# Performance work log

Hardware: AMD Instinct MI355X
Metric: run time of the kernel (lower is better)

## Reference

```python
import jax, jax.numpy as jnp
import numpy as np

# --- config mirroring Prediction(__init__) ---
NUM_CLS = 3        # heatmap channels; total C = NUM_CLS + 2 (offset) + 2 (wh)
TOPK = 100         # peaks kept per stack output
SCALE = 4.0        # scale_factor: feature-map stride
CONF_TH = 0.1      # conf_th (also soft-NMS keep thresh, as in forward())
SIGMA = 0.5        # soft-NMS gaussian sigma (default in soft_nms_pytorch)


def setup_inputs() -> dict:
    key = jax.random.key(0)
    # network is identity => x is the raw head output (B, S, C, H, W)
    x = jax.random.normal(key, (32, 2, NUM_CLS + 4, 256, 256), dtype=jnp.float32)
    return {"x": x}


def _decode(hm, off, wh):
    """CenterNet-style hm2box: hm (C,H,W) post-sigmoid, off/wh (2,H,W)."""
    C, H, W = hm.shape
    scores, idx = jax.lax.top_k(hm.reshape(-1), TOPK)      # over C*H*W
    cls = idx // (H * W)
    rem = idx % (H * W)                                    # spatial flat index
    ys = (rem // W).astype(jnp.float32)
    xs = (rem % W).astype(jnp.float32)
    offx = off[0].reshape(-1)[rem]
    offy = off[1].reshape(-1)[rem]
    bw = wh[0].reshape(-1)[rem] * SCALE
    bh = wh[1].reshape(-1)[rem] * SCALE
    cx = (xs + offx) * SCALE
    cy = (ys + offy) * SCALE
    boxes = jnp.stack([cx - bw / 2, cy - bh / 2, cx + bw / 2, cy + bh / 2], axis=-1)
    # conf_th filter: zero-out low scores (fixed shape stand-in for boolean select)
    scores = jnp.where(scores > CONF_TH, scores, 0.0)
    return boxes, cls, scores


def _soft_nms(boxes, scores):
    """Faithful port of soft_nms_pytorch: sequential max-swap + gaussian decay."""
    N = boxes.shape[0]
    pos = jnp.arange(N)

    def step(carry, i):
        bxs, scs, idxs = carry
        # argmax over scores[i:] (includes i; strict '<' in original == first-max here)
        m = jnp.argmax(jnp.where(pos >= i, scs, -jnp.inf))

        def swap(a):
            ai, am = a[i], a[m]
            return a.at[i].set(am).at[m].set(ai)

        bxs, scs, idxs = swap(bxs), swap(scs), swap(idxs)
        bi = bxs[i]
        x1, y1, x2, y2 = bxs[:, 0], bxs[:, 1], bxs[:, 2], bxs[:, 3]
        areas = (x2 - x1 + 1.0) * (y2 - y1 + 1.0)
        area_i = (bi[2] - bi[0] + 1.0) * (bi[3] - bi[1] + 1.0)
        xx1 = jnp.maximum(bi[0], x1)
        yy1 = jnp.maximum(bi[1], y1)
        xx2 = jnp.minimum(bi[2], x2)
        yy2 = jnp.minimum(bi[3], y2)
        inter = jnp.maximum(0.0, xx2 - xx1 + 1.0) * jnp.maximum(0.0, yy2 - yy1 + 1.0)
        iou = inter / (area_i + areas - inter)
        w = jnp.exp(-(iou * iou) / SIGMA)
        scs = jnp.where(pos > i, w * scs, scs)   # decay only positions after i
        return (bxs, scs, idxs), None

    (bxs, scs, idxs), _ = jax.lax.scan(step, (boxes, scores, jnp.arange(N)), jnp.arange(N))
    keep = scs > CONF_TH
    return bxs, scs, idxs, keep


def reference(x):
    b, s, c, H, W = x.shape
    hm = jax.nn.sigmoid(x[:, :, :NUM_CLS])
    off = x[:, :, NUM_CLS:NUM_CLS + 2]
    wh = x[:, :, NUM_CLS + 2:]
    boxes, clss, scores = jax.vmap(jax.vmap(_decode))(hm, off, wh)
    boxes = boxes.reshape(b, s * TOPK, 4)
    clss = clss.reshape(b, s * TOPK)
    scores = scores.reshape(b, s * TOPK)
    nboxes, nscores, idxs, keep = jax.vmap(_soft_nms)(boxes, scores)
    nclss = jnp.take_along_axis(clss, idxs, axis=1)
    # fixed-shape outputs; `keep` marks the boxes the original would return
    return nboxes, nclss, nscores, keep
```

## Files before the change

kernel.cpp:

```cpp
#include <hip/hip_runtime.h>
#include <math.h>

#define TOPK 100
#define HW 65536
#define SLICE_STRIDE (7*HW)
#define NBATCH 32
#define NBOX 200
#define HM (3*HW)
#define CAP 4096
#define NPART 4
#define PPART 128
#define KEYS_BASE 256
#define WS_NEED ((size_t)(2048 + 64 * NPART * PPART * 8))
#define TKEYS 0xC0400000u

__device__ __forceinline__ unsigned fkey(float f) {
    unsigned u = __float_as_uint(f);
    return (u & 0x80000000u) ? ~u : (u | 0x80000000u);
}

__device__ __forceinline__ float sel4(const float a[4], int s) {
    float r = a[0];
    r = (s == 1) ? a[1] : r;
    r = (s == 2) ? a[2] : r;
    r = (s == 3) ? a[3] : r;
    return r;
}

#if defined(__has_builtin) && __has_builtin(__builtin_amdgcn_update_dpp)
#define DPP64_STEP(ctrl)                                                        \
    {                                                                           \
        unsigned lo = (unsigned)x, hi = (unsigned)(x >> 32);                    \
        unsigned olo = (unsigned)__builtin_amdgcn_update_dpp((int)lo, (int)lo,  \
                                                             (ctrl), 0xF, 0xF, false); \
        unsigned ohi = (unsigned)__builtin_amdgcn_update_dpp((int)hi, (int)hi,  \
                                                             (ctrl), 0xF, 0xF, false); \
        unsigned long long o = ((unsigned long long)ohi << 32) | olo;           \
        x = (o > x) ? o : x;                                                    \
    }
__device__ __forceinline__ unsigned long long wave_umax64(unsigned long long x) {
    DPP64_STEP(0x111)
    DPP64_STEP(0x112)
    DPP64_STEP(0x114)
    DPP64_STEP(0x118)
    DPP64_STEP(0x142)
    DPP64_STEP(0x143)
    unsigned rlo = (unsigned)__builtin_amdgcn_readlane((int)(unsigned)x, 63);
    unsigned rhi = (unsigned)__builtin_amdgcn_readlane((int)(unsigned)(x >> 32), 63);
    return ((unsigned long long)rhi << 32) | rlo;
}
__device__ __forceinline__ float lane_getf(const float a[4], int slot, int lane) {
    return __uint_as_float((unsigned)__builtin_amdgcn_readlane(
        (int)__float_as_uint(sel4(a, slot)), lane));
}
#else
__device__ __forceinline__ unsigned long long wave_umax64(unsigned long long x) {
    #pragma unroll
    for (int off = 32; off > 0; off >>= 1) {
        unsigned long long o = __shfl_xor(x, off);
        if (o > x) x = o;
    }
    return x;
}
__device__ __forceinline__ float lane_getf(const float a[4], int slot, int lane) {
    return __shfl(sel4(a, slot), lane);
}
#endif

__global__ __launch_bounds__(1024) void kcollect(const float* __restrict__ x,
                                                 unsigned long long* __restrict__ ws) {
    __shared__ unsigned shCnt;
    const int bid = blockIdx.x;
    const int slice = bid >> 2, part = bid & 3;
    const int t = threadIdx.x;
    const float* xb = x + (size_t)slice * SLICE_STRIDE;
    const float4* xb4 = (const float4*)xb;
    unsigned* cnt = (unsigned*)ws;
    unsigned long long* keys = ws + KEYS_BASE;

    if (t == 0) shCnt = 0u;
    __syncthreads();

    const int i0 = part * (HM / 4 / NPART);
    const int i1 = i0 + (HM / 4 / NPART);
    for (int i = i0 + t; i < i1; i += 1024) {
        float4 v = xb4[i];
        float a[4] = {v.x, v.y, v.z, v.w};
        #pragma unroll
        for (int q = 0; q < 4; ++q) {
            unsigned vk = fkey(a[q]);
            if (vk >= TKEYS) {
                unsigned pos = atomicAdd(&shCnt, 1u);
                if (pos < PPART)
                    keys[(size_t)slice * (NPART * PPART) + part * PPART + pos] =
                        ((unsigned long long)vk << 32) |
                        (unsigned)~(unsigned)(i * 4 + q);
            }
        }
    }
    __syncthreads();
    if (t == 0) cnt[slice * NPART + part] = shCnt;
}

__device__ void fb_select(const float* xb, unsigned long long* fkrow,
                          unsigned* selmask, float* rv, int* ri, int t) {
    for (int i = t; i < HM / 32; i += 1024) selmask[i] = 0u;
    __syncthreads();
    for (int r = 0; r < TOPK; ++r) {
        float bv = -INFINITY; int bi = 0x7FFFFFFF;
        for (int i = t; i < HM; i += 1024) {
            if (!((selmask[i >> 5] >> (i & 31)) & 1u)) {
                float v = xb[i];
                if (v > bv || (v == bv && i < bi)) { bv = v; bi = i; }
            }
        }
        rv[t] = bv; ri[t] = bi;
        __syncthreads();
        for (int off = 512; off > 0; off >>= 1) {
            if (t < off) {
                float ov = rv[t + off]; int oi = ri[t + off];
                if (ov > rv[t] || (ov == rv[t] && oi < ri[t])) { rv[t] = ov; ri[t] = oi; }
            }
            __syncthreads();
        }
        if (t == 0) {
            int w = ri[0];
            selmask[w >> 5] |= (1u << (w & 31));
            fkrow[r] = ((unsigned long long)fkey(rv[0]) << 32) |
                       (unsigned)~(unsigned)w;
        }
        __syncthreads();
    }
}

__global__ __launch_bounds__(1024) void knms6(const float* __restrict__ x,
                                              const unsigned long long* __restrict__ ws,
                                              float* __restrict__ out) {
    __shared__ unsigned long long shpool64[4096];
    __shared__ unsigned long long fk[2][TOPK];
    __shared__ float4 bxs4[NBOX];
    __shared__ float scs[NBOX];
    __shared__ float cl[NBOX];
    __shared__ int badf[2];

    unsigned long long* skey = shpool64;
    unsigned* selmask = (unsigned*)shpool64;
    float* rv = (float*)(selmask + 6144);
    int* ri = (int*)(selmask + 7168);

    const int b = blockIdx.x, t = threadIdx.x;
    const unsigned* cnt = (const unsigned*)ws;
    const unsigned long long* keys = ws + KEYS_BASE;

    if (t < 2) {
        unsigned tot = 0; int bad = 0;
        for (int p8 = 0; p8 < NPART; ++p8) {
            unsigned c = cnt[(2 * b + t) * NPART + p8];
            tot += c;
            if (c > PPART) bad = 1;
        }
        if (tot < TOPK) bad = 1;
        badf[t] = bad;
    }
    __syncthreads();

    if (badf[0]) fb_select(x + (size_t)(2 * b + 0) * SLICE_STRIDE, fk[0],
                           selmask, rv, ri, t);
    if (badf[1]) fb_select(x + (size_t)(2 * b + 1) * SLICE_STRIDE, fk[1],
                           selmask, rv, ri, t);

    const int half = t >> 9, tt = t & 511;
    const int slice = 2 * b + half;
    {
        int part = tt >> 7, off = tt & 127;
        unsigned c = cnt[slice * NPART + part];
        bool valid = (!badf[half]) && ((unsigned)off < c);
        skey[half * 512 + tt] = valid
            ? keys[(size_t)slice * (NPART * PPART) + part * PPART + off] : 0ull;
    }
    __syncthreads();
    for (int k = 2; k <= 512; k <<= 1) {
        for (int j = k >> 1; j > 0; j >>= 1) {
            int i = tt, ixj = i ^ j;
            if (ixj > i) {
                unsigned long long a = skey[half * 512 + i];
                unsigned long long c2 = skey[half * 512 + ixj];
                bool sw = ((i & k) == 0) ? (a < c2) : (a > c2);
                if (sw) { skey[half * 512 + i] = c2; skey[half * 512 + ixj] = a; }
            }
            __syncthreads();
        }
    }

    if (t < NBOX) {
        const int sB = t / TOPK, rank = t - sB * TOPK;
        const int sl2 = 2 * b + sB;
        unsigned long long K = badf[sB] ? fk[sB][rank] : skey[sB * 512 + rank];
        unsigned vk = (unsigned)(K >> 32);
        unsigned idx = ~((unsigned)K);
        unsigned u = (vk & 0x80000000u) ? (vk & 0x7FFFFFFFu) : ~vk;
        float z = __uint_as_float(u);
        int c = (int)(idx >> 16);
        int rem = (int)(idx & 0xFFFFu);
        const float* xb = x + (size_t)sl2 * SLICE_STRIDE;
        float ysf = (float)(rem >> 8);
        float xsf = (float)(rem & 255);
        float offx = xb[3 * HW + rem];
        float offy = xb[4 * HW + rem];
        float bw = xb[5 * HW + rem] * 4.0f;
        float bh = xb[6 * HW + rem] * 4.0f;
        float cx = (xsf + offx) * 4.0f;
        float cy = (ysf + offy) * 4.0f;
        bxs4[t] = make_float4(cx - bw * 0.5f, cy - bh * 0.5f,
                              cx + bw * 0.5f, cy + bh * 0.5f);
        float sg = 1.0f / (1.0f + expf(-z));
        scs[t] = (sg > 0.1f) ? sg : 0.0f;
        cl[t] = (float)c;
    }
    __syncthreads();

    if (t < 64) {
        float X1[4], Y1[4], X2[4], Y2[4], SC[4], CL4[4], AR[4];
        unsigned CP[4];
        #pragma unroll
        for (int sl = 0; sl < 4; ++sl) {
            int p = sl * 64 + t;
            int q = (p < NBOX) ? p : 0;
            float4 bb = bxs4[q];
            X1[sl] = bb.x; Y1[sl] = bb.y; X2[sl] = bb.z; Y2[sl] = bb.w;
            SC[sl] = (p < NBOX) ? scs[q] : 0.0f;
            CL4[sl] = cl[q];
            CP[sl] = (unsigned)p;
            AR[sl] = (X2[sl] - X1[sl] + 1.0f) * (Y2[sl] - Y1[sl] + 1.0f);
        }

        for (int i = 0; i < NBOX; ++i) {
            const unsigned ui = (unsigned)i;
            unsigned long long loc = 0ull;
            #pragma unroll
            for (int sl = 0; sl < 4; ++sl) {
                unsigned cd = ~((CP[sl] << 8) | (unsigned)(sl * 64 + t));
                unsigned long long k =
                    ((unsigned long long)__float_as_uint(SC[sl]) << 32) | cd;
                if (CP[sl] >= ui && k > loc) loc = k;
            }
            unsigned long long kmax = wave_umax64(loc);

            if ((unsigned)(kmax >> 32) == 0u) break;

            unsigned w32 = ~((unsigned)kmax);
            unsigned m = w32 >> 8;
            int worig = (int)(w32 & 0xFFu);
            int lane_m = worig & 63, slot_m = worig >> 6;

            float pvx1 = lane_getf(X1, slot_m, lane_m);
            float pvy1 = lane_getf(Y1, slot_m, lane_m);
            float pvx2 = lane_getf(X2, slot_m, lane_m);
            float pvy2 = lane_getf(Y2, slot_m, lane_m);
            float area_i = lane_getf(AR, slot_m, lane_m);

            #pragma unroll
            for (int sl = 0; sl < 4; ++sl) {
                unsigned cp = CP[sl];
                unsigned ncp = (cp == ui) ? m : cp;
                ncp = (cp == m) ? ui : ncp;
                CP[sl] = ncp;
            }

            float intr[4]; bool anyp = false;
            #pragma unroll
            for (int sl = 0; sl < 4; ++sl) {
                int p = sl * 64 + t;
                bool act = (p < NBOX) && (CP[sl] > ui);
                float xx1 = fmaxf(pvx1, X1[sl]);
                float yy1 = fmaxf(pvy1, Y1[sl]);
                float xx2 = fminf(pvx2, X2[sl]);
                float yy2 = fminf(pvy2, Y2[sl]);
                float inter = fmaxf(0.0f, xx2 - xx1 + 1.0f) *
                              fmaxf(0.0f, yy2 - yy1 + 1.0f);
                intr[sl] = inter;
                anyp |= (act && inter != 0.0f);
            }
            if (__ballot(anyp) != 0ull) {
                #pragma unroll
                for (int sl = 0; sl < 4; ++sl) {
                    int p = sl * 64 + t;
                    if ((p < NBOX) && (CP[sl] > ui)) {
                        float iou = intr[sl] / (area_i + AR[sl] - intr[sl]);
                        float w = expf(-(iou * iou) / 0.5f);
                        SC[sl] = w * SC[sl];
                    }
                }
            }
        }

        float* ob  = out + (size_t)b * NBOX * 4;
        float* oc  = out + (size_t)NBATCH * NBOX * 4 + b * NBOX;
        float* os  = out + (size_t)NBATCH * NBOX * 5 + b * NBOX;
        float* okp = out + (size_t)NBATCH * NBOX * 6 + b * NBOX;
        #pragma unroll
        for (int sl = 0; sl < 4; ++sl) {
            int p = sl * 64 + t;
            if (p < NBOX) {
                unsigned q = CP[sl];
                ob[q * 4 + 0] = X1[sl];
                ob[q * 4 + 1] = Y1[sl];
                ob[q * 4 + 2] = X2[sl];
                ob[q * 4 + 3] = Y2[sl];
                oc[q]  = CL4[sl];
                os[q]  = SC[sl];
                okp[q] = (SC[sl] > 0.1f) ? 1.0f : 0.0f;
            }
        }
    }
}

__global__ __launch_bounds__(1024) void ktopk(const float* __restrict__ x,
                                              float* __restrict__ out) {
    __shared__ unsigned hist[4096];
    __shared__ unsigned long long cand[CAP];
    __shared__ int shB, shB2;
    __shared__ unsigned shAbove, shNcand, shNc;

    const int slice = blockIdx.x;
    const int b = slice >> 1, s = slice & 1;
    const int t = threadIdx.x;
    const float* xb = x + (size_t)slice * SLICE_STRIDE;
    const float4* xb4 = (const float4*)xb;
    const int N4 = HM / 4;

    if (t == 0) { shB = 0; shB2 = 0; shAbove = 0u; shNcand = 0u; shNc = 0u; }
    for (int i = t; i < 4096; i += 1024) hist[i] = 0u;
    __syncthreads();

    for (int i = t; i < N4; i += 1024) {
        float4 v = xb4[i];
        float a[4] = {v.x, v.y, v.z, v.w};
        #pragma unroll
        for (int c_ = 0; c_ < 4; ++c_) {
            unsigned vk = fkey(a[c_]);
            atomicAdd(&hist[vk >> 20], 1u);
        }
    }
    __syncthreads();

    {
        unsigned* tmp = (unsigned*)cand;
        unsigned* src = hist;
        unsigned* dst = tmp;
        for (int d = 1; d < 4096; d <<= 1) {
            for (int i = t; i < 4096; i += 1024) {
                unsigned v = src[i];
                if (i + d < 4096) v += src[i + d];
                dst[i] = v;
            }
            __syncthreads();
            unsigned* sw = src; src = dst; dst = sw;
        }
        for (int i = t; i < 4096; i += 1024) {
            unsigned sb = src[i];
            unsigned sn = (i < 4095) ? src[i + 1] : 0u;
            if (sb >= TOPK && sn < TOPK) { shB = i; shAbove = sn; shNcand = sb; }
        }
        __syncthreads();
    }

    const bool refine = (shNcand > CAP);
    if (refine) {
        for (int i = t; i < 4096; i += 1024) hist[i] = 0u;
        __syncthreads();
        const unsigned Bv = (unsigned)shB;
        for (int i = t; i < N4; i += 1024) {
            float4 v = xb4[i];
            float a[4] = {v.x, v.y, v.z, v.w};
            #pragma unroll
            for (int c_ = 0; c_ < 4; ++c_) {
                unsigned vk = fkey(a[c_]);
                if ((vk >> 20) == Bv) atomicAdd(&hist[(vk >> 8) & 0xFFFu], 1u);
            }
        }
        __syncthreads();
        if (t == 0) {
            unsigned need = TOPK - shAbove, cum = 0u;
            int b2 = 4095;
            for (; b2 >= 0; --b2) { cum += hist[b2]; if (cum >= need) break; }
            shB2 = (b2 < 0) ? 0 : b2;
            shNcand = shAbove + cum;
        }
        __syncthreads();
    }

    {
        const unsigned Bv = (unsigned)shB;
        const unsigned B2v = refine ? (unsigned)shB2 : 0u;
        for (int i = t; i < N4; i += 1024) {
            float4 v = xb4[i];
            float a[4] = {v.x, v.y, v.z, v.w};
            #pragma unroll
            for (int c_ = 0; c_ < 4; ++c_) {
                unsigned vk = fkey(a[c_]);
                unsigned bin = vk >> 20;
                bool q = refine ? (bin > Bv || (bin == Bv && ((vk >> 8) & 0xFFFu) >= B2v))
                                : (bin >= Bv);
                if (q) {
                    unsigned pos = atomicAdd(&shNc, 1u);
                    if (pos < CAP)
                        cand[pos] = ((unsigned long long)vk << 32) |
                                    (unsigned)~(unsigned)(i * 4 + c_);
                }
            }
        }
        __syncthreads();
    }

    unsigned nc = shNc; if (nc > CAP) nc = CAP;
    int P = 128; while (P < (int)nc) P <<= 1;
    for (int i = (int)nc + t; i < P; i += 1024) cand[i] = 0ull;
    __syncthreads();
    for (int k = 2; k <= P; k <<= 1) {
        for (int j = k >> 1; j > 0; j >>= 1) {
            for (int i = t; i < P; i += 1024) {
                int ixj = i ^ j;
                if (ixj > i) {
                    unsigned long long a = cand[i], c2 = cand[ixj];
                    bool sw = ((i & k) == 0) ? (a < c2) : (a > c2);
                    if (sw) { cand[i] = c2; cand[ixj] = a; }
                }
            }
            __syncthreads();
        }
    }

    if (t < TOPK) {
        unsigned long long K = cand[t];
        unsigned vk = (unsigned)(K >> 32);
        unsigned idx = ~((unsigned)K);
        unsigned u = (vk & 0x80000000u) ? (vk & 0x7FFFFFFFu) : ~vk;
        float z = __uint_as_float(u);
        int c = (int)(idx >> 16);
        int rem = (int)(idx & 0xFFFFu);
        float ysf = (float)(rem >> 8);
        float xsf = (float)(rem & 255);
        float offx = xb[3 * HW + rem];
        float offy = xb[4 * HW + rem];
        float bw = xb[5 * HW + rem] * 4.0f;
        float bh = xb[6 * HW + rem] * 4.0f;
        float cx = (xsf + offx) * 4.0f;
        float cy = (ysf + offy) * 4.0f;
        int slot = s * TOPK + t;
        float* ob = out + (size_t)b * NBOX * 4;
        float* oc = out + (size_t)NBATCH * NBOX * 4 + b * NBOX;
        float* os = out + (size_t)NBATCH * NBOX * 5 + b * NBOX;
        ob[slot * 4 + 0] = cx - bw * 0.5f;
        ob[slot * 4 + 1] = cy - bh * 0.5f;
        ob[slot * 4 + 2] = cx + bw * 0.5f;
        ob[slot * 4 + 3] = cy + bh * 0.5f;
        float sg = 1.0f / (1.0f + expf(-z));
        os[slot] = (sg > 0.1f) ? sg : 0.0f;
        oc[slot] = (float)c;
    }
}

__global__ __launch_bounds__(64) void knms(float* __restrict__ out) {
    __shared__ float bxs[NBOX][4];
    __shared__ float scs[NBOX];
    __shared__ float cl[NBOX];

    const int b = blockIdx.x, t = threadIdx.x;
    float* ob  = out + (size_t)b * NBOX * 4;
    float* oc  = out + (size_t)NBATCH * NBOX * 4 + b * NBOX;
    float* os  = out + (size_t)NBATCH * NBOX * 5 + b * NBOX;
    float* okp = out + (size_t)NBATCH * NBOX * 6 + b * NBOX;

    for (int p = t; p < NBOX; p += 64) {
        bxs[p][0] = ob[p * 4 + 0];
        bxs[p][1] = ob[p * 4 + 1];
        bxs[p][2] = ob[p * 4 + 2];
        bxs[p][3] = ob[p * 4 + 3];
        scs[p] = os[p];
        cl[p]  = oc[p];
    }
    __syncthreads();

    unsigned long long local = 0ull;
    for (int p = t; p < NBOX; p += 64) {
        unsigned long long k =
            ((unsigned long long)__float_as_uint(scs[p]) << 32) | (unsigned)~(unsigned)p;
        if (k > local) local = k;
    }
    #pragma unroll
    for (int off = 32; off > 0; off >>= 1) {
        unsigned long long o = __shfl_xor(local, off);
        if (o > local) local = o;
    }
    unsigned long long kmax = local;

    for (int i = 0; i < NBOX; ++i) {
        int m = (int)(~((unsigned)kmax));
        if (t == 0 && m != i) {
            #pragma unroll
            for (int k = 0; k < 4; ++k) {
                float tmp = bxs[i][k]; bxs[i][k] = bxs[m][k]; bxs[m][k] = tmp;
            }
            float ts = scs[i]; scs[i] = scs[m]; scs[m] = ts;
            float tc = cl[i];  cl[i]  = cl[m];  cl[m]  = tc;
        }
        __syncthreads();

        float b0 = bxs[i][0], b1 = bxs[i][1], b2 = bxs[i][2], b3 = bxs[i][3];
        float area_i = (b2 - b0 + 1.0f) * (b3 - b1 + 1.0f);

        local = 0ull;
        for (int p = i + 1 + t; p < NBOX; p += 64) {
            float x1 = bxs[p][0], y1 = bxs[p][1], x2 = bxs[p][2], y2 = bxs[p][3];
            float areas = (x2 - x1 + 1.0f) * (y2 - y1 + 1.0f);
            float xx1 = fmaxf(b0, x1);
            float yy1 = fmaxf(b1, y1);
            float xx2 = fminf(b2, x2);
            float yy2 = fminf(b3, y2);
            float inter = fmaxf(0.0f, xx2 - xx1 + 1.0f) * fmaxf(0.0f, yy2 - yy1 + 1.0f);
            float iou = inter / (area_i + areas - inter);
            float w = expf(-(iou * iou) / 0.5f);
            float ns = w * scs[p];
            scs[p] = ns;
            unsigned long long k =
                ((unsigned long long)__float_as_uint(ns) << 32) | (unsigned)~(unsigned)p;
            if (k > local) local = k;
        }
        __syncthreads();
        #pragma unroll
        for (int off = 32; off > 0; off >>= 1) {
            unsigned long long o = __shfl_xor(local, off);
            if (o > local) local = o;
        }
        kmax = local;
    }
    __syncthreads();

    for (int p = t; p < NBOX; p += 64) {
        ob[p * 4 + 0] = bxs[p][0];
        ob[p * 4 + 1] = bxs[p][1];
        ob[p * 4 + 2] = bxs[p][2];
        ob[p * 4 + 3] = bxs[p][3];
        oc[p]  = cl[p];
        os[p]  = scs[p];
        okp[p] = (scs[p] > 0.1f) ? 1.0f : 0.0f;
    }
}

extern "C" void kernel_launch(void* const* d_in, const int* in_sizes, int n_in,
                              void* d_out, int out_size, void* d_ws, size_t ws_size,
                              hipStream_t stream) {
    const float* x = (const float*)d_in[0];
    float* out = (float*)d_out;
    if (d_ws != nullptr && ws_size >= WS_NEED) {
        kcollect<<<64 * NPART, 1024, 0, stream>>>(x, (unsigned long long*)d_ws);
        knms6<<<NBATCH, 1024, 0, stream>>>(x, (const unsigned long long*)d_ws, out);
    } else {
        ktopk<<<2 * NBATCH, 1024, 0, stream>>>(x, out);
        knms<<<NBATCH, 64, 0, stream>>>(out);
    }
}
```

Before: 274.3 us.

## Split collection into more partitions and add fast soft-NMS path with overlap precheck

The collection pass is split into 8 partitions of 64 candidates per slice instead of 4 of 128, which doubles the number of collect blocks. The NMS kernel shrinks to 512 threads. It adds a precomputed per-box flag marking boxes that overlap any other box. The sequential soft-NMS loop now uses a 32-bit score max instead of a 64-bit one, writes each selected box out directly instead of tracking permutations, and skips the decay step when the selected box overlaps nothing. If scores tie or reach zero it falls back to the original exact path, at the cost of extra code and a possible double pass.

After: 349.2 us. 1.27x slower.

```diff
diff --git a/kernel.cpp b/kernel.cpp
--- a/kernel.cpp
+++ b/kernel.cpp
@@ -8,8 +8,8 @@
 #define NBOX 200
 #define HM (3*HW)
 #define CAP 4096
-#define NPART 4
-#define PPART 128
+#define NPART 8
+#define PPART 64
 #define KEYS_BASE 256
 #define WS_NEED ((size_t)(2048 + 64 * NPART * PPART * 8))
 #define TKEYS 0xC0400000u
@@ -26,8 +26,26 @@
     r = (s == 3) ? a[3] : r;
     return r;
 }
+__device__ __forceinline__ int sel4i(const int a[4], int s) {
+    int r = a[0];
+    r = (s == 1) ? a[1] : r;
+    r = (s == 2) ? a[2] : r;
+    r = (s == 3) ? a[3] : r;
+    return r;
+}
 
 #if defined(__has_builtin) && __has_builtin(__builtin_amdgcn_update_dpp)
+#define DPP32_STEP(ctrl)                                                        \
+    {                                                                           \
+        unsigned tmp_ = (unsigned)__builtin_amdgcn_update_dpp(                  \
+            (int)x, (int)x, (ctrl), 0xF, 0xF, false);                           \
+        x = x > tmp_ ? x : tmp_;                                                \
+    }
+__device__ __forceinline__ unsigned wave_umax32(unsigned x) {
+    DPP32_STEP(0x111) DPP32_STEP(0x112) DPP32_STEP(0x114)
+    DPP32_STEP(0x118) DPP32_STEP(0x142) DPP32_STEP(0x143)
+    return (unsigned)__builtin_amdgcn_readlane((int)x, 63);
+}
 #define DPP64_STEP(ctrl)                                                        \
     {                                                                           \
         unsigned lo = (unsigned)x, hi = (unsigned)(x >> 32);                    \
@@ -39,21 +57,28 @@
         x = (o > x) ? o : x;                                                    \
     }
 __device__ __forceinline__ unsigned long long wave_umax64(unsigned long long x) {
-    DPP64_STEP(0x111)
-    DPP64_STEP(0x112)
-    DPP64_STEP(0x114)
-    DPP64_STEP(0x118)
-    DPP64_STEP(0x142)
-    DPP64_STEP(0x143)
+    DPP64_STEP(0x111) DPP64_STEP(0x112) DPP64_STEP(0x114)
+    DPP64_STEP(0x118) DPP64_STEP(0x142) DPP64_STEP(0x143)
     unsigned rlo = (unsigned)__builtin_amdgcn_readlane((int)(unsigned)x, 63);
     unsigned rhi = (unsigned)__builtin_amdgcn_readlane((int)(unsigned)(x >> 32), 63);
     return ((unsigned long long)rhi << 32) | rlo;
 }
+__device__ __forceinline__ int lane_geti(int v, int lane) {
+    return __builtin_amdgcn_readlane(v, lane);
+}
 __device__ __forceinline__ float lane_getf(const float a[4], int slot, int lane) {
     return __uint_as_float((unsigned)__builtin_amdgcn_readlane(
         (int)__float_as_uint(sel4(a, slot)), lane));
 }
 #else
+__device__ __forceinline__ unsigned wave_umax32(unsigned x) {
+    #pragma unroll
+    for (int off = 32; off > 0; off >>= 1) {
+        unsigned o = (unsigned)__shfl_xor((int)x, off);
+        x = x > o ? x : o;
+    }
+    return x;
+}
 __device__ __forceinline__ unsigned long long wave_umax64(unsigned long long x) {
     #pragma unroll
     for (int off = 32; off > 0; off >>= 1) {
@@ -62,6 +87,7 @@
     }
     return x;
 }
+__device__ __forceinline__ int lane_geti(int v, int lane) { return __shfl(v, lane); }
 __device__ __forceinline__ float lane_getf(const float a[4], int slot, int lane) {
     return __shfl(sel4(a, slot), lane);
 }
@@ -71,7 +97,7 @@
                                                  unsigned long long* __restrict__ ws) {
     __shared__ unsigned shCnt;
     const int bid = blockIdx.x;
-    const int slice = bid >> 2, part = bid & 3;
+    const int slice = bid >> 3, part = bid & 7;
     const int t = threadIdx.x;
     const float* xb = x + (size_t)slice * SLICE_STRIDE;
     const float4* xb4 = (const float4*)xb;
@@ -104,11 +130,11 @@
 
 __device__ void fb_select(const float* xb, unsigned long long* fkrow,
                           unsigned* selmask, float* rv, int* ri, int t) {
-    for (int i = t; i < HM / 32; i += 1024) selmask[i] = 0u;
+    for (int i = t; i < HM / 32; i += 512) selmask[i] = 0u;
     __syncthreads();
     for (int r = 0; r < TOPK; ++r) {
         float bv = -INFINITY; int bi = 0x7FFFFFFF;
-        for (int i = t; i < HM; i += 1024) {
+        for (int i = t; i < HM; i += 512) {
             if (!((selmask[i >> 5] >> (i & 31)) & 1u)) {
                 float v = xb[i];
                 if (v > bv || (v == bv && i < bi)) { bv = v; bi = i; }
@@ -116,7 +142,7 @@
         }
         rv[t] = bv; ri[t] = bi;
         __syncthreads();
-        for (int off = 512; off > 0; off >>= 1) {
+        for (int off = 256; off > 0; off >>= 1) {
             if (t < off) {
                 float ov = rv[t + off]; int oi = ri[t + off];
                 if (ov > rv[t] || (ov == rv[t] && oi < ri[t])) { rv[t] = ov; ri[t] = oi; }
@@ -133,20 +159,21 @@
     }
 }
 
-__global__ __launch_bounds__(1024) void knms6(const float* __restrict__ x,
-                                              const unsigned long long* __restrict__ ws,
-                                              float* __restrict__ out) {
-    __shared__ unsigned long long shpool64[4096];
+__global__ __launch_bounds__(512) void knms7(const float* __restrict__ x,
+                                             const unsigned long long* __restrict__ ws,
+                                             float* __restrict__ out) {
+    __shared__ unsigned long long shpool64[3584];
     __shared__ unsigned long long fk[2][TOPK];
     __shared__ float4 bxs4[NBOX];
     __shared__ float scs[NBOX];
     __shared__ float cl[NBOX];
+    __shared__ int ovf[NBOX];
     __shared__ int badf[2];
 
     unsigned long long* skey = shpool64;
     unsigned* selmask = (unsigned*)shpool64;
     float* rv = (float*)(selmask + 6144);
-    int* ri = (int*)(selmask + 7168);
+    int* ri = (int*)(selmask + 6656);
 
     const int b = blockIdx.x, t = threadIdx.x;
     const unsigned* cnt = (const unsigned*)ws;
@@ -169,24 +196,26 @@
     if (badf[1]) fb_select(x + (size_t)(2 * b + 1) * SLICE_STRIDE, fk[1],
                            selmask, rv, ri, t);
 
-    const int half = t >> 9, tt = t & 511;
+    const int half = t >> 8, tt = t & 255;
     const int slice = 2 * b + half;
-    {
-        int part = tt >> 7, off = tt & 127;
+    for (int e = tt; e < 512; e += 256) {
+        int part = e >> 6, off = e & 63;
         unsigned c = cnt[slice * NPART + part];
         bool valid = (!badf[half]) && ((unsigned)off < c);
-        skey[half * 512 + tt] = valid
+        skey[half * 512 + e] = valid
             ? keys[(size_t)slice * (NPART * PPART) + part * PPART + off] : 0ull;
     }
     __syncthreads();
     for (int k = 2; k <= 512; k <<= 1) {
         for (int j = k >> 1; j > 0; j >>= 1) {
-            int i = tt, ixj = i ^ j;
-            if (ixj > i) {
-                unsigned long long a = skey[half * 512 + i];
-                unsigned long long c2 = skey[half * 512 + ixj];
-                bool sw = ((i & k) == 0) ? (a < c2) : (a > c2);
-                if (sw) { skey[half * 512 + i] = c2; skey[half * 512 + ixj] = a; }
+            for (int e = tt; e < 512; e += 256) {
+                int i = e, ixj = i ^ j;
+                if (ixj > i) {
+                    unsigned long long a = skey[half * 512 + i];
+                    unsigned long long c2 = skey[half * 512 + ixj];
+                    bool sw = ((i & k) == 0) ? (a < c2) : (a > c2);
+                    if (sw) { skey[half * 512 + i] = c2; skey[half * 512 + ixj] = a; }
+                }
             }
             __syncthreads();
         }
@@ -219,9 +248,24 @@
     }
     __syncthreads();
 
+    if (t < NBOX) {
+        float4 me = bxs4[t];
+        int ov = 0;
+        for (int q = 0; q < NBOX; ++q) {
+            if (q == t) continue;
+            float4 o = bxs4[q];
+            float gx = fminf(me.z, o.z) - fmaxf(me.x, o.x) + 1.0f;
+            float gy = fminf(me.w, o.w) - fmaxf(me.y, o.y) + 1.0f;
+            if (gx > 0.0f && gy > 0.0f) { ov = 1; break; }
+        }
+        ovf[t] = ov;
+    }
+    __syncthreads();
+
     if (t < 64) {
         float X1[4], Y1[4], X2[4], Y2[4], SC[4], CL4[4], AR[4];
-        unsigned CP[4];
+        unsigned KB[4]; int OV4[4];
+        unsigned selb = 0u;
         #pragma unroll
         for (int sl = 0; sl < 4; ++sl) {
             int p = sl * 64 + t;
@@ -230,86 +274,156 @@
             X1[sl] = bb.x; Y1[sl] = bb.y; X2[sl] = bb.z; Y2[sl] = bb.w;
             SC[sl] = (p < NBOX) ? scs[q] : 0.0f;
             CL4[sl] = cl[q];
-            CP[sl] = (unsigned)p;
             AR[sl] = (X2[sl] - X1[sl] + 1.0f) * (Y2[sl] - Y1[sl] + 1.0f);
-        }
-
-        for (int i = 0; i < NBOX; ++i) {
-            const unsigned ui = (unsigned)i;
-            unsigned long long loc = 0ull;
-            #pragma unroll
-            for (int sl = 0; sl < 4; ++sl) {
-                unsigned cd = ~((CP[sl] << 8) | (unsigned)(sl * 64 + t));
-                unsigned long long k =
-                    ((unsigned long long)__float_as_uint(SC[sl]) << 32) | cd;
-                if (CP[sl] >= ui && k > loc) loc = k;
-            }
-            unsigned long long kmax = wave_umax64(loc);
-
-            if ((unsigned)(kmax >> 32) == 0u) break;
-
-            unsigned w32 = ~((unsigned)kmax);
-            unsigned m = w32 >> 8;
-            int worig = (int)(w32 & 0xFFu);
-            int lane_m = worig & 63, slot_m = worig >> 6;
-
-            float pvx1 = lane_getf(X1, slot_m, lane_m);
-            float pvy1 = lane_getf(Y1, slot_m, lane_m);
-            float pvx2 = lane_getf(X2, slot_m, lane_m);
-            float pvy2 = lane_getf(Y2, slot_m, lane_m);
-            float area_i = lane_getf(AR, slot_m, lane_m);
-
-            #pragma unroll
-            for (int sl = 0; sl < 4; ++sl) {
-                unsigned cp = CP[sl];
-                unsigned ncp = (cp == ui) ? m : cp;
-                ncp = (cp == m) ? ui : ncp;
-                CP[sl] = ncp;
-            }
-
-            float intr[4]; bool anyp = false;
-            #pragma unroll
-            for (int sl = 0; sl < 4; ++sl) {
-                int p = sl * 64 + t;
-                bool act = (p < NBOX) && (CP[sl] > ui);
-                float xx1 = fmaxf(pvx1, X1[sl]);
-                float yy1 = fmaxf(pvy1, Y1[sl]);
-                float xx2 = fminf(pvx2, X2[sl]);
-                float yy2 = fminf(pvy2, Y2[sl]);
-                float inter = fmaxf(0.0f, xx2 - xx1 + 1.0f) *
-                              fmaxf(0.0f, yy2 - yy1 + 1.0f);
-                intr[sl] = inter;
-                anyp |= (act && inter != 0.0f);
-            }
-            if (__ballot(anyp) != 0ull) {
-                #pragma unroll
-                for (int sl = 0; sl < 4; ++sl) {
-                    int p = sl * 64 + t;
-                    if ((p < NBOX) && (CP[sl] > ui)) {
-                        float iou = intr[sl] / (area_i + AR[sl] - intr[sl]);
-                        float w = expf(-(iou * iou) / 0.5f);
-                        SC[sl] = w * SC[sl];
-                    }
-                }
-            }
+            KB[sl] = (p < NBOX) ? __float_as_uint(SC[sl]) : 0u;
+            OV4[sl] = (p < NBOX) ? ovf[q] : 0;
+            if (p >= NBOX) selb |= (1u << sl);
         }
 
         float* ob  = out + (size_t)b * NBOX * 4;
         float* oc  = out + (size_t)NBATCH * NBOX * 4 + b * NBOX;
         float* os  = out + (size_t)NBATCH * NBOX * 5 + b * NBOX;
         float* okp = out + (size_t)NBATCH * NBOX * 6 + b * NBOX;
-        #pragma unroll
-        for (int sl = 0; sl < 4; ++sl) {
-            int p = sl * 64 + t;
-            if (p < NBOX) {
-                unsigned q = CP[sl];
-                ob[q * 4 + 0] = X1[sl];
-                ob[q * 4 + 1] = Y1[sl];
-                ob[q * 4 + 2] = X2[sl];
-                ob[q * 4 + 3] = Y2[sl];
-                oc[q]  = CL4[sl];
-                os[q]  = SC[sl];
-                okp[q] = (SC[sl] > 0.1f) ? 1.0f : 0.0f;
+
+        bool fb = false;
+        for (int i = 0; i < NBOX; ++i) {
+            unsigned lb = KB[0] > KB[1] ? KB[0] : KB[1];
+            unsigned lb2 = KB[2] > KB[3] ? KB[2] : KB[3];
+            lb = lb > lb2 ? lb : lb2;
+            unsigned smax = wave_umax32(lb);
+            if (smax == 0u) { fb = true; break; }
+
+            unsigned long long mk = __ballot(lb == smax);
+            if (__popcll(mk) > 1ull) { fb = true; break; }
+            int wl = (int)__builtin_ctzll(mk);
+            int nm = (KB[0] == smax) + (KB[1] == smax) +
+                     (KB[2] == smax) + (KB[3] == smax);
+            int fs = 3;
+            fs = (KB[2] == smax) ? 2 : fs;
+            fs = (KB[1] == smax) ? 1 : fs;
+            fs = (KB[0] == smax) ? 0 : fs;
+            if (lane_geti(nm, wl) > 1) { fb = true; break; }
+            int ws_ = lane_geti(fs, wl);
+            int wov = lane_geti(sel4i(OV4, ws_), wl);
+
+            if (t == wl) {
+                selb |= (1u << ws_);
+                #pragma unroll
+                for (int sl = 0; sl < 4; ++sl) if (sl == ws_) KB[sl] = 0u;
+                float4 bb = make_float4(sel4(X1, ws_), sel4(Y1, ws_),
+                                        sel4(X2, ws_), sel4(Y2, ws_));
+                *(float4*)(ob + (size_t)i * 4) = bb;
+                float bsc = sel4(SC, ws_);
+                oc[i]  = sel4(CL4, ws_);
+                os[i]  = bsc;
+                okp[i] = (bsc > 0.1f) ? 1.0f : 0.0f;
+            }
+
+            if (wov) {
+                float pvx1 = lane_getf(X1, ws_, wl);
+                float pvy1 = lane_getf(Y1, ws_, wl);
+                float pvx2 = lane_getf(X2, ws_, wl);
+                float pvy2 = lane_getf(Y2, ws_, wl);
+                float area_i = lane_getf(AR, ws_, wl);
+                #pragma unroll
+                for (int sl = 0; sl < 4; ++sl) {
+                    if (!((selb >> sl) & 1u)) {
+                        float xx1 = fmaxf(pvx1, X1[sl]);
+                        float yy1 = fmaxf(pvy1, Y1[sl]);
+                        float xx2 = fminf(pvx2, X2[sl]);
+                        float yy2 = fminf(pvy2, Y2[sl]);
+                        float inter = fmaxf(0.0f, xx2 - xx1 + 1.0f) *
+                                      fmaxf(0.0f, yy2 - yy1 + 1.0f);
+                        float iou = inter / (area_i + AR[sl] - inter);
+                        float w = expf(-(iou * iou) / 0.5f);
+                        SC[sl] = w * SC[sl];
+                        KB[sl] = __float_as_uint(SC[sl]);
+                    }
+                }
+            }
+        }
+
+        if (fb) {
+            float aX1[4], aY1[4], aX2[4], aY2[4], aSC[4], aCL[4], aAR[4];
+            unsigned CP[4];
+            #pragma unroll
+            for (int sl = 0; sl < 4; ++sl) {
+                int p = sl * 64 + t;
+                int q = (p < NBOX) ? p : 0;
+                float4 bb = bxs4[q];
+                aX1[sl] = bb.x; aY1[sl] = bb.y; aX2[sl] = bb.z; aY2[sl] = bb.w;
+                aSC[sl] = (p < NBOX) ? scs[q] : 0.0f;
+                aCL[sl] = cl[q];
+                CP[sl] = (unsigned)p;
+                aAR[sl] = (aX2[sl] - aX1[sl] + 1.0f) * (aY2[sl] - aY1[sl] + 1.0f);
+            }
+            for (int i = 0; i < NBOX; ++i) {
+                const unsigned ui = (unsigned)i;
+                unsigned long long loc = 0ull;
+                #pragma unroll
+                for (int sl = 0; sl < 4; ++sl) {
+                    unsigned cd = ~((CP[sl] << 8) | (unsigned)(sl * 64 + t));
+                    unsigned long long k =
+                        ((unsigned long long)__float_as_uint(aSC[sl]) << 32) | cd;
+                    if (CP[sl] >= ui && k > loc) loc = k;
+                }
+                unsigned long long kmax = wave_umax64(loc);
+                if ((unsigned)(kmax >> 32) == 0u) break;
+                unsigned w32 = ~((unsigned)kmax);
+                unsigned m = w32 >> 8;
+                int worig = (int)(w32 & 0xFFu);
+                int lane_m = worig & 63, slot_m = worig >> 6;
+                float pvx1 = lane_getf(aX1, slot_m, lane_m);
+                float pvy1 = lane_getf(aY1, slot_m, lane_m);
+                float pvx2 = lane_getf(aX2, slot_m, lane_m);
+                float pvy2 = lane_getf(aY2, slot_m, lane_m);
+                float area_i = lane_getf(aAR, slot_m, lane_m);
+                #pragma unroll
+                for (int sl = 0; sl < 4; ++sl) {
+                    unsigned cp = CP[sl];
+                    unsigned ncp = (cp == ui) ? m : cp;
+                    ncp = (cp == m) ? ui : ncp;
+                    CP[sl] = ncp;
+                }
+                float intr[4]; bool anyp = false;
+                #pragma unroll
+                for (int sl = 0; sl < 4; ++sl) {
+                    int p = sl * 64 + t;
+                    bool act = (p < NBOX) && (CP[sl] > ui);
+                    float xx1 = fmaxf(pvx1, aX1[sl]);
+                    float yy1 = fmaxf(pvy1, aY1[sl]);
+                    float xx2 = fminf(pvx2, aX2[sl]);
+                    float yy2 = fminf(pvy2, aY2[sl]);
+                    float inter = fmaxf(0.0f, xx2 - xx1 + 1.0f) *
+                                  fmaxf(0.0f, yy2 - yy1 + 1.0f);
+                    intr[sl] = inter;
+                    anyp |= (act && inter != 0.0f);
+                }
+                if (__ballot(anyp) != 0ull) {
+                    #pragma unroll
+                    for (int sl = 0; sl < 4; ++sl) {
+                        int p = sl * 64 + t;
+                        if ((p < NBOX) && (CP[sl] > ui)) {
+                            float iou = intr[sl] / (area_i + aAR[sl] - intr[sl]);
+                            float w = expf(-(iou * iou) / 0.5f);
+                            aSC[sl] = w * aSC[sl];
+                        }
+                    }
+                }
+            }
+            #pragma unroll
+            for (int sl = 0; sl < 4; ++sl) {
+                int p = sl * 64 + t;
+                if (p < NBOX) {
+                    unsigned q = CP[sl];
+                    ob[q * 4 + 0] = aX1[sl];
+                    ob[q * 4 + 1] = aY1[sl];
+                    ob[q * 4 + 2] = aX2[sl];
+                    ob[q * 4 + 3] = aY2[sl];
+                    oc[q]  = aCL[sl];
+                    os[q]  = aSC[sl];
+                    okp[q] = (aSC[sl] > 0.1f) ? 1.0f : 0.0f;
+                }
             }
         }
     }
@@ -555,7 +669,7 @@
     float* out = (float*)d_out;
     if (d_ws != nullptr && ws_size >= WS_NEED) {
         kcollect<<<64 * NPART, 1024, 0, stream>>>(x, (unsigned long long*)d_ws);
-        knms6<<<NBATCH, 1024, 0, stream>>>(x, (const unsigned long long*)d_ws, out);
+        knms7<<<NBATCH, 512, 0, stream>>>(x, (const unsigned long long*)d_ws, out);
     } else {
         ktopk<<<2 * NBATCH, 1024, 0, stream>>>(x, out);
         knms<<<NBATCH, 64, 0, stream>>>(out);
```
